# Optimization experiments

Hardware: AMD Instinct MI355X
Metric: run time of the kernel (lower is better)

## Reference

```python
import jax, jax.numpy as jnp
import numpy as np

NX = 48
N_TILES = 6
C_IN = 16
H = 32            # node_hidden_channels
EH = 64           # edge_hidden_channels
N_STEPS = 4       # num_step_message_passing
N_NODES = N_TILES * NX * NX


def _build_edges(nx, n_tiles):
    # 4-neighbor (up/down/left/right, wraparound) connectivity per tile
    ii = np.arange(nx * nx, dtype=np.int32).reshape(nx, nx)
    srcs, dsts = [], []
    for t in range(n_tiles):
        off = t * nx * nx
        for ax, sh in ((0, 1), (0, -1), (1, 1), (1, -1)):
            srcs.append(off + np.roll(ii, sh, axis=ax).ravel())
            dsts.append(off + ii.ravel())
    return np.concatenate(srcs), np.concatenate(dsts)


def setup_inputs() -> dict:
    key = jax.random.key(0)
    ks = jax.random.split(key, 16)
    src_np, dst_np = _build_edges(NX, N_TILES)
    E = src_np.shape[0]  # 55296
    s = 0.1
    return {
        "in_node_feats": jax.random.normal(ks[0], (2, N_TILES, NX, NX, C_IN), jnp.float32),
        "edge_feats": jax.random.normal(ks[1], (E, 2), jnp.float32),
        "src": jnp.asarray(src_np, jnp.int32),
        "dst": jnp.asarray(dst_np, jnp.int32),
        # project_node_feats: Linear(C_IN,H) -> relu -> Linear(H,H)
        "pW1": jax.random.normal(ks[2], (C_IN, H), jnp.float32) * s,
        "pb1": jnp.zeros((H,), jnp.float32),
        "pW2": jax.random.normal(ks[3], (H, H), jnp.float32) * s,
        "pb2": jnp.zeros((H,), jnp.float32),
        # edge network: Linear(2,EH) -> relu -> Linear(EH, H*H)
        "eW1": jax.random.normal(ks[4], (2, EH), jnp.float32) * s,
        "eb1": jnp.zeros((EH,), jnp.float32),
        "eW2": jax.random.normal(ks[5], (EH, H * H), jnp.float32) * (s / 4.0),
        "eb2": jnp.zeros((H * H,), jnp.float32),
        # NNConv bias
        "conv_b": jnp.zeros((H,), jnp.float32),
        # GRU (single layer): gate order r, z, n (PyTorch)
        "gWih": jax.random.normal(ks[6], (3 * H, H), jnp.float32) * s,
        "gWhh": jax.random.normal(ks[7], (3 * H, H), jnp.float32) * s,
        "gbih": jnp.zeros((3 * H,), jnp.float32),
        "gbhh": jnp.zeros((3 * H,), jnp.float32),
    }


def reference(in_node_feats, edge_feats, src, dst,
              pW1, pb1, pW2, pb2, eW1, eb1, eW2, eb2,
              conv_b, gWih, gWhh, gbih, gbhh):
    shp = in_node_feats.shape           # (B, T, nx, ny, Cin)
    B = shp[0]
    N = shp[1] * shp[2] * shp[3]
    x = in_node_feats.reshape(B, N, shp[-1])
    # project node features
    x = jnp.maximum(x @ pW1 + pb1, 0.0) @ pW2 + pb2      # (B, N, H)
    # per-edge weight matrices (shared across batch and steps)
    We = jnp.maximum(edge_feats @ eW1 + eb1, 0.0) @ eW2 + eb2
    We = We.reshape(-1, H, H)                             # (E, H, H)
    h = x
    seg = jax.vmap(lambda m: jax.ops.segment_sum(m, dst, num_segments=N))
    for _ in range(N_STEPS):
        # NNConv: gather src feats, per-edge matmul, scatter-sum to dst, + bias
        msg = jnp.einsum('beh,eho->beo', x[:, src], We)   # (B, E, H)
        x = jnp.maximum(seg(msg) + conv_b, 0.0)           # relu(conv)
        # GRU cell (seq_len = 1)
        gx = x @ gWih.T + gbih
        gh = h @ gWhh.T + gbhh
        xr, xz, xn = jnp.split(gx, 3, axis=-1)
        hr, hz, hn = jnp.split(gh, 3, axis=-1)
        r = jax.nn.sigmoid(xr + hr)
        z = jax.nn.sigmoid(xz + hz)
        n = jnp.tanh(xn + r * hn)
        h = (1.0 - z) * n + z * h
        x = h
    return x.reshape(shp[:4] + (H,))
```

## Files before the change

kernel.cpp:

```cpp
#include <hip/hip_runtime.h>
#include <stdint.h>

constexpr int NB   = 2;
constexpr int NN   = 13824;
constexpr int NE   = 55296;
constexpr int H    = 32;
constexpr int EHID = 64;
constexpr int HH   = 1024;
constexpr int TILE = 2304;
constexpr int NXC  = 48;

typedef float f32x4 __attribute__((ext_vector_type(4)));
typedef short s16x8 __attribute__((ext_vector_type(8)));
typedef unsigned int u32x2 __attribute__((ext_vector_type(2)));
typedef unsigned int u32x4 __attribute__((ext_vector_type(4)));
typedef __attribute__((address_space(1))) unsigned int as1_uint;
typedef __attribute__((address_space(3))) unsigned int as3_uint;

static __device__ __forceinline__ unsigned short f2bf(float f) {
    unsigned u = __float_as_uint(f);
    return (unsigned short)((u + 0x7fffu + ((u >> 16) & 1u)) >> 16);
}
static __device__ __forceinline__ unsigned packbf(float lo, float hi) {
    return (unsigned)f2bf(lo) | ((unsigned)f2bf(hi) << 16);
}
static __device__ __forceinline__ void gload16(const void* g, void* l) {
    __builtin_amdgcn_global_load_lds((const as1_uint*)g, (as3_uint*)l, 16, 0, 0);
}
static __device__ __forceinline__ float sigf(float v) {
    return 1.0f / (1.0f + __expf(-v));
}
static __device__ __forceinline__ float tanhfast(float v) {
    return 1.0f - 2.0f / (1.0f + __expf(2.0f * v));
}

__global__ void __launch_bounds__(256)
k_prep(const float* __restrict__ ef, const float* __restrict__ eW1,
       const float* __restrict__ eb1, unsigned short* __restrict__ aB,
       const float* __restrict__ eW2, const float* __restrict__ eb2,
       unsigned short* __restrict__ BpT, float* __restrict__ eb2p) {
    int blk = blockIdx.x;
    if (blk < 3456) {
        int t = blk * 256 + threadIdx.x;
        int e = t >> 4, kq = (t & 15) * 4;
        float f0 = ef[e * 2], f1 = ef[e * 2 + 1];
        u32x2 w;
#pragma unroll
        for (int q = 0; q < 2; q++) {
            int k = kq + q * 2;
            float v0 = fmaxf(f0 * eW1[k]     + f1 * eW1[64 + k]     + eb1[k],     0.f);
            float v1 = fmaxf(f0 * eW1[k + 1] + f1 * eW1[64 + k + 1] + eb1[k + 1], 0.f);
            w[q] = packbf(v0, v1);
        }
        *(u32x2*)(aB + e * 64 + kq) = w;
    } else {
        int t = (blk - 3456) * 256 + threadIdx.x;
        int jp = t >> 4, kq = (t & 15) * 4;
        int src_col = (jp & 31) * 32 + (jp >> 5);
        u32x2 w;
#pragma unroll
        for (int q = 0; q < 2; q++) {
            int k = kq + q * 2;
            w[q] = packbf(eW2[k * HH + src_col], eW2[(k + 1) * HH + src_col]);
        }
        *(u32x2*)(BpT + jp * 64 + kq) = w;
        if (kq == 0) eb2p[jp] = eb2[src_col];
    }
}

__global__ void __launch_bounds__(256)
k_gemm(const unsigned short* __restrict__ Bp, const unsigned short* __restrict__ Ae,
       const float* __restrict__ eb2p, unsigned short* __restrict__ C) {
    __shared__ unsigned char lds[32768] __attribute__((aligned(16)));
    const int tid  = threadIdx.x;
    const int wv   = tid >> 6;
    const int lane = tid & 63;
    const int lr   = lane & 15;
    const int lg   = lane >> 4;
    const int jbt  = blockIdx.x;
    const int ebt  = blockIdx.y;

    const unsigned char* Ag = (const unsigned char*)Bp + (size_t)jbt * 16384;
    const unsigned char* Bg = (const unsigned char*)Ae + (size_t)ebt * 16384;

#pragma unroll
    for (int c = 0; c < 4; c++) {
        int fbase = (wv * 4 + c) * 1024;
        int f  = fbase + lane * 16;
        int sw = f ^ (((f >> 7) & 7) << 4);
        gload16(Ag + sw, lds + fbase);
        gload16(Bg + sw, lds + 16384 + fbase);
    }
    asm volatile("s_waitcnt vmcnt(0)" ::: "memory");
    __syncthreads();

    const int wm = wv >> 1, wn = wv & 1;
    f32x4 acc[4][4] = {};
#pragma unroll
    for (int kk = 0; kk < 2; kk++) {
        s16x8 af[4], bf[4];
#pragma unroll
        for (int i = 0; i < 4; i++) {
            int la = ((wm * 64 + i * 16 + lr) * 64 + kk * 32 + lg * 8) * 2;
            la ^= ((la >> 7) & 7) << 4;
            af[i] = *(const s16x8*)(lds + la);
            int lb = ((wn * 64 + i * 16 + lr) * 64 + kk * 32 + lg * 8) * 2;
            lb ^= ((lb >> 7) & 7) << 4;
            bf[i] = *(const s16x8*)(lds + 16384 + lb);
        }
#pragma unroll
        for (int i = 0; i < 4; i++)
#pragma unroll
            for (int j = 0; j < 4; j++)
                acc[i][j] = __builtin_amdgcn_mfma_f32_16x16x32_bf16(af[i], bf[j], acc[i][j], 0, 0, 0);
    }

    float bias[4][4];
#pragma unroll
    for (int i = 0; i < 4; i++)
#pragma unroll
        for (int r = 0; r < 4; r++)
            bias[i][r] = eb2p[jbt * 128 + wm * 64 + i * 16 + lg * 4 + r];

    __syncthreads();
#pragma unroll
    for (int i = 0; i < 4; i++) {
#pragma unroll
        for (int j = 0; j < 4; j++) {
            int el    = wn * 64 + j * 16 + lr;
            int jbase = wm * 64 + i * 16 + lg * 4;
            int L0 = el * 256 + jbase * 2;
            int ph = L0 ^ ((el & 7) << 4);
            u32x2 w;
            w[0] = packbf(acc[i][j][0] + bias[i][0], acc[i][j][1] + bias[i][1]);
            w[1] = packbf(acc[i][j][2] + bias[i][2], acc[i][j][3] + bias[i][3]);
            *(u32x2*)(lds + ph) = w;
        }
    }
    __syncthreads();

    const size_t cbase = (size_t)(ebt * 128) * 2048 + (size_t)jbt * 256;
#pragma unroll
    for (int pass = 0; pass < 8; pass++) {
        int L2 = pass * 4096 + tid * 16;
        int el = L2 >> 8;
        int ph = L2 ^ ((el & 7) << 4);
        u32x4 v = *(const u32x4*)(lds + ph);
        *(u32x4*)((unsigned char*)C + cbase + (size_t)el * 2048 + (L2 & 255)) = v;
    }
}

__global__ void __launch_bounds__(256)
k_proj(const float* __restrict__ in, const float* __restrict__ pW1,
       const float* __restrict__ pb1, const float* __restrict__ pW2,
       const float* __restrict__ pb2, float* __restrict__ S0,
       unsigned short* __restrict__ xb0,
       const float* __restrict__ gWih, const float* __restrict__ gWhh,
       unsigned short* __restrict__ gWb) {
    int blk = blockIdx.x;
    if (blk >= 3456) {
        int idx = (blk - 3456) * 256 + threadIdx.x;
        gWb[idx] = f2bf(idx < 3072 ? gWih[idx] : gWhh[idx - 3072]);
        return;
    }
    int t = blk * 256 + threadIdx.x;
    int p = t >> 5;
    int l = t & 31;
    float iv = (l < 16) ? in[p * 16 + l] : 0.f;
    float hid = pb1[l];
#pragma unroll
    for (int c = 0; c < 16; c++) hid = fmaf(__shfl(iv, c, 32), pW1[c * H + l], hid);
    hid = fmaxf(hid, 0.f);
    float out = pb2[l];
#pragma unroll
    for (int h = 0; h < 32; h++) out = fmaf(__shfl(hid, h, 32), pW2[h * H + l], out);
    S0[p * H + l]  = out;
    xb0[p * H + l] = f2bf(out);
}

__global__ void __launch_bounds__(256)
k_step2(const unsigned short* __restrict__ xb_in,
        const float* __restrict__ h_in,
        const unsigned short* __restrict__ WeT,
        const float* __restrict__ conv_b,
        const unsigned short* __restrict__ gWb,
        const float* __restrict__ gbih, const float* __restrict__ gbhh,
        float* __restrict__ h_out, unsigned short* __restrict__ xb_out) {
    __shared__ unsigned short cv[2][16][32];
    const int tid  = threadIdx.x;
    const int wv   = tid >> 6;
    const int l    = tid & 63;
    const int cl   = l & 15;
    const int kg   = l >> 4;
    const int bsel = cl & 1;
    const int n0   = blockIdx.x * 16;

    f32x4 cb0 = *(const f32x4*)(conv_b + kg * 4);
    f32x4 cb1 = *(const f32x4*)(conv_b + 16 + kg * 4);

    for (int u = 0; u < 4; ++u) {
        int n = n0 + wv * 4 + u;
        int t = n / TILE;
        int i = n - t * TILE;
        int r = i / NXC;
        int c = i - r * NXC;
        int bt = t * TILE;
        int rm = (r == 0) ? NXC - 1 : r - 1;
        int rp = (r == NXC - 1) ? 0 : r + 1;
        int cm = (c == 0) ? NXC - 1 : c - 1;
        int cp = (c == NXC - 1) ? 0 : c + 1;
        int ss[4] = {bt + rm * NXC + c, bt + rp * NXC + c,
                     bt + r * NXC + cm, bt + r * NXC + cp};

        f32x4 a0 = {}, a1 = {};
#pragma unroll
        for (int k = 0; k < 4; ++k) {
            size_t e = (size_t)((t * 4 + k) * TILE + i);
            const unsigned short* wp = WeT + e * HH;
            s16x8 af0 = *(const s16x8*)(wp + cl * 32 + kg * 8);
            s16x8 af1 = *(const s16x8*)(wp + 512 + cl * 32 + kg * 8);
            s16x8 bfr = *(const s16x8*)(xb_in + ((size_t)(bsel * NN + ss[k])) * 32 + kg * 8);
            a0 = __builtin_amdgcn_mfma_f32_16x16x32_bf16(af0, bfr, a0, 0, 0, 0);
            a1 = __builtin_amdgcn_mfma_f32_16x16x32_bf16(af1, bfr, a1, 0, 0, 0);
        }
        if (cl < 2) {
            int nl = wv * 4 + u;
            unsigned* cp32 = (unsigned*)&cv[cl][nl][0];
            cp32[kg * 2]     = packbf(fmaxf(a0[0] + cb0[0], 0.f), fmaxf(a0[1] + cb0[1], 0.f));
            cp32[kg * 2 + 1] = packbf(fmaxf(a0[2] + cb0[2], 0.f), fmaxf(a0[3] + cb0[3], 0.f));
            cp32[8 + kg * 2]     = packbf(fmaxf(a1[0] + cb1[0], 0.f), fmaxf(a1[1] + cb1[1], 0.f));
            cp32[8 + kg * 2 + 1] = packbf(fmaxf(a1[2] + cb1[2], 0.f), fmaxf(a1[3] + cb1[3], 0.f));
        }
    }
    __syncthreads();

    if (wv < 2) {
        const int b = wv;
        const size_t mbase = (size_t)b * NN + n0;

        s16x8 ax = *(const s16x8*)&cv[b][cl][kg * 8];
        s16x8 ah = *(const s16x8*)(xb_in + (mbase + cl) * 32 + kg * 8);

        f32x4 accx[6], acch[6];
#pragma unroll
        for (int jb = 0; jb < 6; ++jb) {
            s16x8 wx = *(const s16x8*)(gWb + (jb * 16 + cl) * 32 + kg * 8);
            s16x8 wh = *(const s16x8*)(gWb + 3072 + (jb * 16 + cl) * 32 + kg * 8);
            f32x4 z0 = {};
            f32x4 z1 = {};
            accx[jb] = __builtin_amdgcn_mfma_f32_16x16x32_bf16(ax, wx, z0, 0, 0, 0);
            acch[jb] = __builtin_amdgcn_mfma_f32_16x16x32_bf16(ah, wh, z1, 0, 0, 0);
        }

        float bihR[2] = {gbih[cl],      gbih[16 + cl]};
        float bihZ[2] = {gbih[32 + cl], gbih[48 + cl]};
        float bihN[2] = {gbih[64 + cl], gbih[80 + cl]};
        float bhhR[2] = {gbhh[cl],      gbhh[16 + cl]};
        float bhhZ[2] = {gbhh[32 + cl], gbhh[48 + cl]};
        float bhhN[2] = {gbhh[64 + cl], gbhh[80 + cl]};

#pragma unroll
        for (int hb = 0; hb < 2; ++hb) {
            const float* hp = h_in  + mbase * 32 + kg * 128 + hb * 16 + cl;
            float*       op = h_out + mbase * 32 + kg * 128 + hb * 16 + cl;
            unsigned short* xp = xb_out + mbase * 32 + kg * 128 + hb * 16 + cl;
#pragma unroll
            for (int ri = 0; ri < 4; ++ri) {
                float rg = sigf(accx[hb][ri] + acch[hb][ri] + bihR[hb] + bhhR[hb]);
                float zg = sigf(accx[2 + hb][ri] + acch[2 + hb][ri] + bihZ[hb] + bhhZ[hb]);
                float ng = tanhfast((accx[4 + hb][ri] + bihN[hb]) +
                                    rg * (acch[4 + hb][ri] + bhhN[hb]));
                float ho = hp[ri * 32];
                float hn = fmaf(zg, ho - ng, ng);
                op[ri * 32] = hn;
                xp[ri * 32] = f2bf(hn);
            }
        }
    }
}

extern "C" void kernel_launch(void* const* d_in, const int* in_sizes, int n_in,
                              void* d_out, int out_size, void* d_ws, size_t ws_size,
                              hipStream_t stream) {
    const float* in_nodes = (const float*)d_in[0];
    const float* ef       = (const float*)d_in[1];
    const float* pW1      = (const float*)d_in[4];
    const float* pb1      = (const float*)d_in[5];
    const float* pW2      = (const float*)d_in[6];
    const float* pb2      = (const float*)d_in[7];
    const float* eW1      = (const float*)d_in[8];
    const float* eb1      = (const float*)d_in[9];
    const float* eW2      = (const float*)d_in[10];
    const float* eb2      = (const float*)d_in[11];
    const float* convb    = (const float*)d_in[12];
    const float* gWih     = (const float*)d_in[13];
    const float* gWhh     = (const float*)d_in[14];
    const float* gbih     = (const float*)d_in[15];
    const float* gbhh     = (const float*)d_in[16];

    unsigned char* ws = (unsigned char*)d_ws;
    unsigned short* WeT  = (unsigned short*)(ws + 0ull);
    unsigned short* aB   = (unsigned short*)(ws + 113246208ull);
    unsigned short* xb0  = (unsigned short*)(ws + 113246208ull);
    unsigned short* xb1  = (unsigned short*)(ws + 115015680ull);
    unsigned short* gWb  = (unsigned short*)(ws + 118554624ull);
    unsigned short* BpT  = (unsigned short*)(ws + 120324096ull);
    float*          eb2p = (float*)         (ws + 120455168ull);
    float*          S0   = (float*)         (ws + 120459264ull);
    float*          S1   = (float*)         (ws + 123998208ull);

    k_prep<<<3456 + 64, 256, 0, stream>>>(ef, eW1, eb1, aB, eW2, eb2, BpT, eb2p);
    dim3 g3(8, 432);
    k_gemm<<<g3, 256, 0, stream>>>(BpT, aB, eb2p, WeT);
    k_proj<<<3456 + 24, 256, 0, stream>>>(in_nodes, pW1, pb1, pW2, pb2, S0, xb0,
                                          gWih, gWhh, gWb);

    float* out = (float*)d_out;
    k_step2<<<864, 256, 0, stream>>>(xb0, S0, WeT, convb, gWb, gbih, gbhh, S1, xb1);
    k_step2<<<864, 256, 0, stream>>>(xb1, S1, WeT, convb, gWb, gbih, gbhh, S0, xb0);
    k_step2<<<864, 256, 0, stream>>>(xb0, S0, WeT, convb, gWb, gbih, gbhh, S1, xb1);
    k_step2<<<864, 256, 0, stream>>>(xb1, S1, WeT, convb, gWb, gbih, gbhh, out, xb0);
}
```

Before: 219.3 us.

## Store edge weights node-major, merge prep kernels, halve per-block node count

The GEMM epilogue now writes per-edge weight matrices in node-major order, so the four incoming edges of each node sit next to each other. The step kernel can then load all of a node's weights up front from contiguous memory before the MFMAs run. The projection and GRU weight conversion kernels are folded into the prep kernel, removing one launch, and the xb/gWb buffers are moved so they no longer alias aB. Each step block now handles 8 nodes instead of 16, which doubles the grid, and only one wave runs the GRU. That adds register pressure from the preloaded fragments and leaves the block underused during the GRU phase.

```diff
diff --git a/kernel.cpp b/kernel.cpp
--- a/kernel.cpp
+++ b/kernel.cpp
@@ -35,10 +35,16 @@
 }
 
 __global__ void __launch_bounds__(256)
-k_prep(const float* __restrict__ ef, const float* __restrict__ eW1,
-       const float* __restrict__ eb1, unsigned short* __restrict__ aB,
-       const float* __restrict__ eW2, const float* __restrict__ eb2,
-       unsigned short* __restrict__ BpT, float* __restrict__ eb2p) {
+k_pre(const float* __restrict__ ef, const float* __restrict__ eW1,
+      const float* __restrict__ eb1, unsigned short* __restrict__ aB,
+      const float* __restrict__ eW2, const float* __restrict__ eb2,
+      unsigned short* __restrict__ BpT, float* __restrict__ eb2p,
+      const float* __restrict__ in, const float* __restrict__ pW1,
+      const float* __restrict__ pb1, const float* __restrict__ pW2,
+      const float* __restrict__ pb2, float* __restrict__ S0,
+      unsigned short* __restrict__ xb0,
+      const float* __restrict__ gWih, const float* __restrict__ gWhh,
+      unsigned short* __restrict__ gWb) {
     int blk = blockIdx.x;
     if (blk < 3456) {
         int t = blk * 256 + threadIdx.x;
@@ -53,7 +59,7 @@
             w[q] = packbf(v0, v1);
         }
         *(u32x2*)(aB + e * 64 + kq) = w;
-    } else {
+    } else if (blk < 3520) {
         int t = (blk - 3456) * 256 + threadIdx.x;
         int jp = t >> 4, kq = (t & 15) * 4;
         int src_col = (jp & 31) * 32 + (jp >> 5);
@@ -65,6 +71,23 @@
         }
         *(u32x2*)(BpT + jp * 64 + kq) = w;
         if (kq == 0) eb2p[jp] = eb2[src_col];
+    } else if (blk < 6976) {
+        int t = (blk - 3520) * 256 + threadIdx.x;
+        int p = t >> 5;
+        int l = t & 31;
+        float iv = (l < 16) ? in[p * 16 + l] : 0.f;
+        float hid = pb1[l];
+#pragma unroll
+        for (int c = 0; c < 16; c++) hid = fmaf(__shfl(iv, c, 32), pW1[c * H + l], hid);
+        hid = fmaxf(hid, 0.f);
+        float out = pb2[l];
+#pragma unroll
+        for (int h = 0; h < 32; h++) out = fmaf(__shfl(hid, h, 32), pW2[h * H + l], out);
+        S0[p * H + l]  = out;
+        xb0[p * H + l] = f2bf(out);
+    } else {
+        int idx = (blk - 6976) * 256 + threadIdx.x;
+        gWb[idx] = f2bf(idx < 3072 ? gWih[idx] : gWhh[idx - 3072]);
     }
 }
 
@@ -139,67 +162,42 @@
     }
     __syncthreads();
 
-    const size_t cbase = (size_t)(ebt * 128) * 2048 + (size_t)jbt * 256;
+    const int q  = (ebt * 128) / TILE;
+    const int i0 = (ebt * 128) % TILE;
+    const int tt = q >> 2, kk2 = q & 3;
+    const size_t nbase = (size_t)tt * TILE + i0;
 #pragma unroll
     for (int pass = 0; pass < 8; pass++) {
         int L2 = pass * 4096 + tid * 16;
         int el = L2 >> 8;
         int ph = L2 ^ ((el & 7) << 4);
         u32x4 v = *(const u32x4*)(lds + ph);
-        *(u32x4*)((unsigned char*)C + cbase + (size_t)el * 2048 + (L2 & 255)) = v;
+        size_t drow = (nbase + el) * 4 + kk2;
+        *(u32x4*)((unsigned char*)C + drow * 2048 + (size_t)jbt * 256 + (L2 & 255)) = v;
     }
 }
 
 __global__ void __launch_bounds__(256)
-k_proj(const float* __restrict__ in, const float* __restrict__ pW1,
-       const float* __restrict__ pb1, const float* __restrict__ pW2,
-       const float* __restrict__ pb2, float* __restrict__ S0,
-       unsigned short* __restrict__ xb0,
-       const float* __restrict__ gWih, const float* __restrict__ gWhh,
-       unsigned short* __restrict__ gWb) {
-    int blk = blockIdx.x;
-    if (blk >= 3456) {
-        int idx = (blk - 3456) * 256 + threadIdx.x;
-        gWb[idx] = f2bf(idx < 3072 ? gWih[idx] : gWhh[idx - 3072]);
-        return;
-    }
-    int t = blk * 256 + threadIdx.x;
-    int p = t >> 5;
-    int l = t & 31;
-    float iv = (l < 16) ? in[p * 16 + l] : 0.f;
-    float hid = pb1[l];
-#pragma unroll
-    for (int c = 0; c < 16; c++) hid = fmaf(__shfl(iv, c, 32), pW1[c * H + l], hid);
-    hid = fmaxf(hid, 0.f);
-    float out = pb2[l];
-#pragma unroll
-    for (int h = 0; h < 32; h++) out = fmaf(__shfl(hid, h, 32), pW2[h * H + l], out);
-    S0[p * H + l]  = out;
-    xb0[p * H + l] = f2bf(out);
-}
-
-__global__ void __launch_bounds__(256)
-k_step2(const unsigned short* __restrict__ xb_in,
+k_step3(const unsigned short* __restrict__ xb_in,
         const float* __restrict__ h_in,
-        const unsigned short* __restrict__ WeT,
+        const unsigned short* __restrict__ WeTn,
         const float* __restrict__ conv_b,
         const unsigned short* __restrict__ gWb,
         const float* __restrict__ gbih, const float* __restrict__ gbhh,
         float* __restrict__ h_out, unsigned short* __restrict__ xb_out) {
-    __shared__ unsigned short cv[2][16][32];
+    __shared__ unsigned short cv[2][8][32];
     const int tid  = threadIdx.x;
     const int wv   = tid >> 6;
     const int l    = tid & 63;
     const int cl   = l & 15;
     const int kg   = l >> 4;
     const int bsel = cl & 1;
-    const int n0   = blockIdx.x * 16;
-
-    f32x4 cb0 = *(const f32x4*)(conv_b + kg * 4);
-    f32x4 cb1 = *(const f32x4*)(conv_b + 16 + kg * 4);
-
-    for (int u = 0; u < 4; ++u) {
-        int n = n0 + wv * 4 + u;
+    const int n0   = blockIdx.x * 8;
+
+    int srcs[2][4];
+#pragma unroll
+    for (int un = 0; un < 2; ++un) {
+        int n = n0 + wv * 2 + un;
         int t = n / TILE;
         int i = n - t * TILE;
         int r = i / NXC;
@@ -209,37 +207,52 @@
         int rp = (r == NXC - 1) ? 0 : r + 1;
         int cm = (c == 0) ? NXC - 1 : c - 1;
         int cp = (c == NXC - 1) ? 0 : c + 1;
-        int ss[4] = {bt + rm * NXC + c, bt + rp * NXC + c,
-                     bt + r * NXC + cm, bt + r * NXC + cp};
-
-        f32x4 a0 = {}, a1 = {};
+        srcs[un][0] = bt + rm * NXC + c;
+        srcs[un][1] = bt + rp * NXC + c;
+        srcs[un][2] = bt + r * NXC + cm;
+        srcs[un][3] = bt + r * NXC + cp;
+    }
+
+    s16x8 af[2][4][2];
+#pragma unroll
+    for (int un = 0; un < 2; ++un) {
+        const unsigned short* wp = WeTn + ((size_t)(n0 + wv * 2 + un) * 4) * HH;
 #pragma unroll
         for (int k = 0; k < 4; ++k) {
-            size_t e = (size_t)((t * 4 + k) * TILE + i);
-            const unsigned short* wp = WeT + e * HH;
-            s16x8 af0 = *(const s16x8*)(wp + cl * 32 + kg * 8);
-            s16x8 af1 = *(const s16x8*)(wp + 512 + cl * 32 + kg * 8);
-            s16x8 bfr = *(const s16x8*)(xb_in + ((size_t)(bsel * NN + ss[k])) * 32 + kg * 8);
-            a0 = __builtin_amdgcn_mfma_f32_16x16x32_bf16(af0, bfr, a0, 0, 0, 0);
-            a1 = __builtin_amdgcn_mfma_f32_16x16x32_bf16(af1, bfr, a1, 0, 0, 0);
-        }
-        if (cl < 2) {
-            int nl = wv * 4 + u;
+            af[un][k][0] = *(const s16x8*)(wp + k * HH + cl * 32 + kg * 8);
+            af[un][k][1] = *(const s16x8*)(wp + k * HH + 512 + cl * 32 + kg * 8);
+        }
+    }
+
+    f32x4 a[2][2] = {};
+#pragma unroll
+    for (int un = 0; un < 2; ++un) {
+#pragma unroll
+        for (int k = 0; k < 4; ++k) {
+            s16x8 bfr = *(const s16x8*)(xb_in + ((size_t)(bsel * NN + srcs[un][k])) * 32 + kg * 8);
+            a[un][0] = __builtin_amdgcn_mfma_f32_16x16x32_bf16(af[un][k][0], bfr, a[un][0], 0, 0, 0);
+            a[un][1] = __builtin_amdgcn_mfma_f32_16x16x32_bf16(af[un][k][1], bfr, a[un][1], 0, 0, 0);
+        }
+    }
+
+    f32x4 cb0 = *(const f32x4*)(conv_b + kg * 4);
+    f32x4 cb1 = *(const f32x4*)(conv_b + 16 + kg * 4);
+    if (cl < 2) {
+#pragma unroll
+        for (int un = 0; un < 2; ++un) {
+            int nl = wv * 2 + un;
             unsigned* cp32 = (unsigned*)&cv[cl][nl][0];
-            cp32[kg * 2]     = packbf(fmaxf(a0[0] + cb0[0], 0.f), fmaxf(a0[1] + cb0[1], 0.f));
-            cp32[kg * 2 + 1] = packbf(fmaxf(a0[2] + cb0[2], 0.f), fmaxf(a0[3] + cb0[3], 0.f));
-            cp32[8 + kg * 2]     = packbf(fmaxf(a1[0] + cb1[0], 0.f), fmaxf(a1[1] + cb1[1], 0.f));
-            cp32[8 + kg * 2 + 1] = packbf(fmaxf(a1[2] + cb1[2], 0.f), fmaxf(a1[3] + cb1[3], 0.f));
+            cp32[kg * 2]     = packbf(fmaxf(a[un][0][0] + cb0[0], 0.f), fmaxf(a[un][0][1] + cb0[1], 0.f));
+            cp32[kg * 2 + 1] = packbf(fmaxf(a[un][0][2] + cb0[2], 0.f), fmaxf(a[un][0][3] + cb0[3], 0.f));
+            cp32[8 + kg * 2]     = packbf(fmaxf(a[un][1][0] + cb1[0], 0.f), fmaxf(a[un][1][1] + cb1[1], 0.f));
+            cp32[8 + kg * 2 + 1] = packbf(fmaxf(a[un][1][2] + cb1[2], 0.f), fmaxf(a[un][1][3] + cb1[3], 0.f));
         }
     }
     __syncthreads();
 
-    if (wv < 2) {
-        const int b = wv;
-        const size_t mbase = (size_t)b * NN + n0;
-
-        s16x8 ax = *(const s16x8*)&cv[b][cl][kg * 8];
-        s16x8 ah = *(const s16x8*)(xb_in + (mbase + cl) * 32 + kg * 8);
+    if (wv == 0) {
+        s16x8 ax = *(const s16x8*)&cv[cl >> 3][cl & 7][kg * 8];
+        s16x8 ah = *(const s16x8*)(xb_in + ((size_t)(cl >> 3) * NN + n0 + (cl & 7)) * 32 + kg * 8);
 
         f32x4 accx[6], acch[6];
 #pragma unroll
@@ -261,19 +274,18 @@
 
 #pragma unroll
         for (int hb = 0; hb < 2; ++hb) {
-            const float* hp = h_in  + mbase * 32 + kg * 128 + hb * 16 + cl;
-            float*       op = h_out + mbase * 32 + kg * 128 + hb * 16 + cl;
-            unsigned short* xp = xb_out + mbase * 32 + kg * 128 + hb * 16 + cl;
 #pragma unroll
             for (int ri = 0; ri < 4; ++ri) {
+                int rrow = kg * 4 + ri;
+                size_t m = (size_t)(rrow >> 3) * NN + n0 + (rrow & 7);
                 float rg = sigf(accx[hb][ri] + acch[hb][ri] + bihR[hb] + bhhR[hb]);
                 float zg = sigf(accx[2 + hb][ri] + acch[2 + hb][ri] + bihZ[hb] + bhhZ[hb]);
                 float ng = tanhfast((accx[4 + hb][ri] + bihN[hb]) +
                                     rg * (acch[4 + hb][ri] + bhhN[hb]));
-                float ho = hp[ri * 32];
+                float ho = h_in[m * 32 + hb * 16 + cl];
                 float hn = fmaf(zg, ho - ng, ng);
-                op[ri * 32] = hn;
-                xp[ri * 32] = f2bf(hn);
+                h_out[m * 32 + hb * 16 + cl]  = hn;
+                xb_out[m * 32 + hb * 16 + cl] = f2bf(hn);
             }
         }
     }
@@ -299,25 +311,25 @@
     const float* gbhh     = (const float*)d_in[16];
 
     unsigned char* ws = (unsigned char*)d_ws;
-    unsigned short* WeT  = (unsigned short*)(ws + 0ull);
+    unsigned short* WeTn = (unsigned short*)(ws + 0ull);
     unsigned short* aB   = (unsigned short*)(ws + 113246208ull);
-    unsigned short* xb0  = (unsigned short*)(ws + 113246208ull);
-    unsigned short* xb1  = (unsigned short*)(ws + 115015680ull);
-    unsigned short* gWb  = (unsigned short*)(ws + 118554624ull);
     unsigned short* BpT  = (unsigned short*)(ws + 120324096ull);
     float*          eb2p = (float*)         (ws + 120455168ull);
     float*          S0   = (float*)         (ws + 120459264ull);
     float*          S1   = (float*)         (ws + 123998208ull);
-
-    k_prep<<<3456 + 64, 256, 0, stream>>>(ef, eW1, eb1, aB, eW2, eb2, BpT, eb2p);
+    unsigned short* xb0  = (unsigned short*)(ws + 127537152ull);
+    unsigned short* xb1  = (unsigned short*)(ws + 129306624ull);
+    unsigned short* gWb  = (unsigned short*)(ws + 131076096ull);
+
+    k_pre<<<7000, 256, 0, stream>>>(ef, eW1, eb1, aB, eW2, eb2, BpT, eb2p,
+                                    in_nodes, pW1, pb1, pW2, pb2, S0, xb0,
+                                    gWih, gWhh, gWb);
     dim3 g3(8, 432);
-    k_gemm<<<g3, 256, 0, stream>>>(BpT, aB, eb2p, WeT);
-    k_proj<<<3456 + 24, 256, 0, stream>>>(in_nodes, pW1, pb1, pW2, pb2, S0, xb0,
-                                          gWih, gWhh, gWb);
+    k_gemm<<<g3, 256, 0, stream>>>(BpT, aB, eb2p, WeTn);
 
     float* out = (float*)d_out;
-    k_step2<<<864, 256, 0, stream>>>(xb0, S0, WeT, convb, gWb, gbih, gbhh, S1, xb1);
-    k_step2<<<864, 256, 0, stream>>>(xb1, S1, WeT, convb, gWb, gbih, gbhh, S0, xb0);
-    k_step2<<<864, 256, 0, stream>>>(xb0, S0, WeT, convb, gWb, gbih, gbhh, S1, xb1);
-    k_step2<<<864, 256, 0, stream>>>(xb1, S1, WeT, convb, gWb, gbih, gbhh, out, xb0);
-}
+    k_step3<<<1728, 256, 0, stream>>>(xb0, S0, WeTn, convb, gWb, gbih, gbhh, S1, xb1);
+    k_step3<<<1728, 256, 0, stream>>>(xb1, S1, WeTn, convb, gWb, gbih, gbhh, S0, xb0);
+    k_step3<<<1728, 256, 0, stream>>>(xb0, S0, WeTn, convb, gWb, gbih, gbhh, S1, xb1);
+    k_step3<<<1728, 256, 0, stream>>>(xb1, S1, WeTn, convb, gWb, gbih, gbhh, out, xb0);
+}
```

After: 217.7 us. About the same (-0.7%).
